# Optimization experiments

Measured on AMD Instinct MI355X. Metric: run time of the kernel, lower is better.

The kernel has to match this reference:

```python
import jax, jax.numpy as jnp
import numpy as np

EPS = 1e-8  # RMSNormMultiHead default eps (forward passes self.eps)


def rms_norm_multihead(x, weight):
    # x: (B, L, H, d); normalize over last dim in float32, then scale per (H, d)
    x32 = x.astype(jnp.float32)
    normed = x32 * jax.lax.rsqrt(jnp.mean(x32 * x32, axis=-1, keepdims=True) + EPS)
    return normed.astype(x.dtype) * weight


def setup_inputs() -> dict:
    key = jax.random.key(0)
    k0, k1, k2 = jax.random.split(key, 3)
    B, L, D, H = 2, 1024, 1024, 16
    d = D // H
    X = jax.random.normal(k0, (B, L, D), dtype=jnp.float32)
    Wq = jax.random.normal(k1, (D, D), dtype=jnp.float32) * 0.02  # q_proj weight (out, in)
    Wv = jax.random.normal(k2, (D, D), dtype=jnp.float32) * 0.02  # v_proj weight (out, in)
    q_norm_w = jnp.ones((H, d), dtype=jnp.float32)
    v_norm_w = jnp.ones((H, d), dtype=jnp.float32)
    return {"X": X, "Wq": Wq, "Wv": Wv, "q_norm_w": q_norm_w, "v_norm_w": v_norm_w}


def reference(X, Wq, Wv, q_norm_w, v_norm_w):
    B, L, D = X.shape
    H, d = q_norm_w.shape
    K = X.reshape(B, L, H, d)
    Q = rms_norm_multihead((X @ Wq.T).reshape(B, L, H, d), q_norm_w)
    V = rms_norm_multihead((X @ Wv.T).reshape(B, L, H, d), v_norm_w)
    # cumulative outer-product KV state: (B, L, H, d, e)
    W = jnp.cumsum(jnp.einsum('blhd,blhe->blhde', K, V), axis=1)
    out = jnp.einsum('blhd,blhde->blhe', Q, W).reshape(B, L, D)
    return out
```

## Files before the change

### kernel.cpp

```cpp
#include <hip/hip_runtime.h>

#define BB 2
#define LL 1024
#define DD 1024
#define HH 16
#define NC 16
#define EPSF 1e-8f

typedef __attribute__((ext_vector_type(8))) short bf16x8;
typedef __attribute__((ext_vector_type(4))) float f32x4;
typedef unsigned short u16;

static __device__ inline u16 f2bf(float f) {
    unsigned int u = __builtin_bit_cast(unsigned int, f);
    u += 0x7fff + ((u >> 16) & 1);
    return (u16)(u >> 16);
}
static __device__ inline float bf2f(u16 v) {
    unsigned int u = ((unsigned int)v) << 16;
    return __builtin_bit_cast(float, u);
}
static __device__ inline void gload_lds16(const u16* g, u16* l) {
    __builtin_amdgcn_global_load_lds((const __attribute__((address_space(1))) void*)g,
                                     (__attribute__((address_space(3))) void*)l, 16, 0, 0);
}

__global__ __launch_bounds__(256) void cvt_k(const float* __restrict__ X,
                                             const float* __restrict__ Wq,
                                             const float* __restrict__ Wv,
                                             u16* __restrict__ Xb,
                                             u16* __restrict__ Wqb,
                                             u16* __restrict__ Wvb)
{
    int i = (blockIdx.x * 256 + threadIdx.x) * 4;
    const float* s; u16* d; int off;
    if (i < 2*1024*1024)      { s = X;  d = Xb;  off = i; }
    else if (i < 3*1024*1024) { s = Wq; d = Wqb; off = i - 2*1024*1024; }
    else                      { s = Wv; d = Wvb; off = i - 3*1024*1024; }
    float4 v = *(const float4*)(s + off);
    ushort4 o;
    o.x = f2bf(v.x); o.y = f2bf(v.y); o.z = f2bf(v.z); o.w = f2bf(v.w);
    *(ushort4*)(d + off) = o;
}

__global__ __launch_bounds__(256) void gemm_fused(const u16* __restrict__ Xb,
                                                  const u16* __restrict__ Wqb,
                                                  const u16* __restrict__ Wvb,
                                                  const float* __restrict__ qw,
                                                  const float* __restrict__ vw,
                                                  u16* __restrict__ Qb,
                                                  u16* __restrict__ Vb,
                                                  u16* __restrict__ S)
{
    const int K = DD, N = DD;
    const u16* W = blockIdx.z ? Wvb : Wqb;
    const float* nw = blockIdx.z ? vw : qw;
    u16* Y = blockIdx.z ? Vb : Qb;
    __shared__ u16 As0[128 * 32], As1[128 * 32];
    __shared__ u16 Bs0[64 * 32],  Bs1[64 * 32];
    __shared__ u16 Vt[64][136];
    __shared__ u16 Kt[64][136];

    const int tid = threadIdx.x, w = tid >> 6, lane = tid & 63;
    const int quad = lane >> 4, l16 = lane & 15;
    const int m0 = blockIdx.y * 128, n0 = blockIdx.x * 64;
    const int lrow = lane >> 2;
    const int lcol = ((lane & 3) ^ ((lane >> 3) & 3)) * 8;

    const u16* gA0 = Xb + (size_t)(m0 + w*16 + lrow) * K + lcol;
    const u16* gA1 = gA0 + (size_t)64 * K;
    const u16* gB0 = W + (size_t)(n0 + w*16 + lrow) * K + lcol;
    u16* lA0_0 = &As0[(w*16) * 32];      u16* lA0_1 = &As1[(w*16) * 32];
    u16* lA1_0 = &As0[(64 + w*16) * 32]; u16* lA1_1 = &As1[(64 + w*16) * 32];
    u16* lB0_0 = &Bs0[(w*16) * 32];      u16* lB0_1 = &Bs1[(w*16) * 32];

    const int sw = (quad ^ ((l16 >> 1) & 3)) * 8;

    f32x4 acc[2][4] = {};
    for (int k0 = 0; k0 < K; k0 += 64) {
        gload_lds16(gA0 + k0,      lA0_0);
        gload_lds16(gA0 + k0 + 32, lA0_1);
        gload_lds16(gA1 + k0,      lA1_0);
        gload_lds16(gA1 + k0 + 32, lA1_1);
        gload_lds16(gB0 + k0,      lB0_0);
        gload_lds16(gB0 + k0 + 32, lB0_1);
        __syncthreads();
        #pragma unroll
        for (int hh = 0; hh < 2; ++hh) {
            const u16* Ah = hh ? As1 : As0;
            const u16* Bh = hh ? Bs1 : Bs0;
            bf16x8 af[2], bfr[4];
            #pragma unroll
            for (int i = 0; i < 2; ++i)
                af[i] = *(const bf16x8*)&Ah[(w*32 + i*16 + l16) * 32 + sw];
            #pragma unroll
            for (int j = 0; j < 4; ++j)
                bfr[j] = *(const bf16x8*)&Bh[(j*16 + l16) * 32 + sw];
            #pragma unroll
            for (int i = 0; i < 2; ++i)
                #pragma unroll
                for (int j = 0; j < 4; ++j)
                    acc[i][j] = __builtin_amdgcn_mfma_f32_16x16x32_bf16(af[i], bfr[j], acc[i][j], 0, 0, 0);
        }
        __syncthreads();
    }

    float wv4[4];
    #pragma unroll
    for (int j = 0; j < 4; ++j) wv4[j] = nw[n0 + j*16 + l16];
    #pragma unroll
    for (int i = 0; i < 2; ++i) {
        float ss[4];
        #pragma unroll
        for (int r = 0; r < 4; ++r) {
            float s = 0.f;
            #pragma unroll
            for (int j = 0; j < 4; ++j) s += acc[i][j][r] * acc[i][j][r];
            ss[r] = s;
        }
        #pragma unroll
        for (int off = 1; off < 16; off <<= 1)
            #pragma unroll
            for (int r = 0; r < 4; ++r) ss[r] += __shfl_xor(ss[r], off, 64);
        float sc[4];
        #pragma unroll
        for (int r = 0; r < 4; ++r) sc[r] = rsqrtf(ss[r] * (1.f/64.f) + EPSF);
        #pragma unroll
        for (int r = 0; r < 4; ++r) {
            u16* yp = Y + (size_t)(m0 + w*32 + i*16 + quad*4 + r) * N + n0;
            #pragma unroll
            for (int j = 0; j < 4; ++j) {
                u16 val = f2bf(acc[i][j][r] * sc[r] * wv4[j]);
                yp[j*16 + l16] = val;
                if (blockIdx.z)
                    Vt[j*16 + l16][w*32 + i*16 + quad*4 + r] = val;
            }
        }
    }

    if (blockIdx.z) {
        {
            const int row = tid >> 1, q2 = tid & 1;
            size_t gb = (size_t)(m0 + row) * DD + n0 + q2 * 32;
            u16 kk[32];
            #pragma unroll
            for (int i2 = 0; i2 < 32; i2 += 4)
                *(ushort4*)&kk[i2] = *(const ushort4*)(Xb + gb + i2);
            #pragma unroll
            for (int i2 = 0; i2 < 32; ++i2)
                Kt[q2*32 + i2][row] = kk[i2];
        }
        __syncthreads();
        const int me = (w & 1) * 32, nd = (w >> 1) * 32;
        const int b = m0 >> 10, c0 = (m0 & 1023) >> 6, h = blockIdx.x;
        const int bh = b * HH + h;
        #pragma unroll
        for (int cc = 0; cc < 2; ++cc) {
            f32x4 sacc[2][2] = {};
            #pragma unroll
            for (int k0 = 0; k0 < 64; k0 += 32) {
                bf16x8 av[2], bv[2];
                #pragma unroll
                for (int i2 = 0; i2 < 2; ++i2)
                    av[i2] = *(const bf16x8*)&Vt[me + i2*16 + l16][cc*64 + k0 + quad*8];
                #pragma unroll
                for (int j2 = 0; j2 < 2; ++j2)
                    bv[j2] = *(const bf16x8*)&Kt[nd + j2*16 + l16][cc*64 + k0 + quad*8];
                #pragma unroll
                for (int i2 = 0; i2 < 2; ++i2)
                    #pragma unroll
                    for (int j2 = 0; j2 < 2; ++j2)
                        sacc[i2][j2] = __builtin_amdgcn_mfma_f32_16x16x32_bf16(av[i2], bv[j2], sacc[i2][j2], 0, 0, 0);
            }
            u16* Sp = S + ((size_t)((bh << 4) | (c0 + cc)) << 12) + w*1024;
            #pragma unroll
            for (int i2 = 0; i2 < 2; ++i2)
                #pragma unroll
                for (int j2 = 0; j2 < 2; ++j2)
                    #pragma unroll
                    for (int r = 0; r < 4; ++r)
                        Sp[(i2*2 + j2)*256 + r*64 + lane] = f2bf(sacc[i2][j2][r]);
        }
    }
}

__global__ __launch_bounds__(256) void out_k2(const u16* __restrict__ Xb,
                                              const u16* __restrict__ Qb,
                                              const u16* __restrict__ Vb,
                                              const u16* __restrict__ S,
                                              float* __restrict__ out)
{
    const int c = 15 - (blockIdx.x & 15);
    const int bh = blockIdx.x >> 4;
    const int h = bh & 15, b = bh >> 4;
    __shared__ u16 Qs[64][72];
    __shared__ u16 Ks[64][72];
    __shared__ u16 Vt[64][72];
    __shared__ u16 St[64][72];
    const int tid = threadIdx.x;
    {
        const int row = tid >> 2, q = tid & 3;
        size_t gbase = (size_t)(b*LL + c*64 + row) * DD + h*64 + q*16;
        u16 vv[16];
        #pragma unroll
        for (int i = 0; i < 16; i += 4) {
            *(ushort4*)&Qs[row][q*16 + i] = *(const ushort4*)(Qb + gbase + i);
            *(ushort4*)&Ks[row][q*16 + i] = *(const ushort4*)(Xb + gbase + i);
            *(ushort4*)&vv[i] = *(const ushort4*)(Vb + gbase + i);
        }
        #pragma unroll
        for (int i = 0; i < 16; ++i)
            Vt[q*16 + i][row] = vv[i];
        float facc[16] = {};
        const u16* Sbase = S + ((size_t)(bh * NC) << 12);
        int cp = 0;
        for (; cp + 2 <= c; cp += 2) {
            const u16* Sc0 = Sbase + ((size_t)cp << 12);
            const u16* Sc1 = Sc0 + 4096;
            #pragma unroll
            for (int jj = 0; jj < 4; ++jj) {
                ushort4 sv0 = *(const ushort4*)(Sc0 + tid*4 + jj*1024);
                ushort4 sv1 = *(const ushort4*)(Sc1 + tid*4 + jj*1024);
                facc[jj*4+0] += bf2f(sv0.x); facc[jj*4+0] += bf2f(sv1.x);
                facc[jj*4+1] += bf2f(sv0.y); facc[jj*4+1] += bf2f(sv1.y);
                facc[jj*4+2] += bf2f(sv0.z); facc[jj*4+2] += bf2f(sv1.z);
                facc[jj*4+3] += bf2f(sv0.w); facc[jj*4+3] += bf2f(sv1.w);
            }
        }
        if (cp < c) {
            const u16* Sc = Sbase + ((size_t)cp << 12);
            #pragma unroll
            for (int jj = 0; jj < 4; ++jj) {
                ushort4 sv = *(const ushort4*)(Sc + tid*4 + jj*1024);
                facc[jj*4+0] += bf2f(sv.x);
                facc[jj*4+1] += bf2f(sv.y);
                facc[jj*4+2] += bf2f(sv.z);
                facc[jj*4+3] += bf2f(sv.w);
            }
        }
        #pragma unroll
        for (int jj = 0; jj < 4; ++jj) {
            int g = tid * 4;
            int ij = (g >> 8) & 3, r = (g >> 6) & 3, ln = g & 63;
            int e = (jj & 1)*32 + (ij >> 1)*16 + (ln >> 4)*4 + r;
            int d = (jj >> 1)*32 + (ij & 1)*16 + (ln & 15);
            ushort4 o;
            o.x = f2bf(facc[jj*4+0]);
            o.y = f2bf(facc[jj*4+1]);
            o.z = f2bf(facc[jj*4+2]);
            o.w = f2bf(facc[jj*4+3]);
            *(ushort4*)&St[e][d] = o;
        }
    }
    __syncthreads();
    const int w = tid >> 6, lane = tid & 63, quad = lane >> 4, l16 = lane & 15;
    const int mo = (w & 1) * 32, no = (w >> 1) * 32;

    f32x4 pacc[2][2] = {};
    #pragma unroll
    for (int k0 = 0; k0 < 64; k0 += 32) {
        bf16x8 aq[2], bk[2];
        #pragma unroll
        for (int i = 0; i < 2; ++i)
            aq[i] = *(const bf16x8*)&Qs[mo + i*16 + l16][k0 + quad*8];
        #pragma unroll
        for (int j = 0; j < 2; ++j)
            bk[j] = *(const bf16x8*)&Ks[no + j*16 + l16][k0 + quad*8];
        #pragma unroll
        for (int i = 0; i < 2; ++i)
            #pragma unroll
            for (int j = 0; j < 2; ++j)
                pacc[i][j] = __builtin_amdgcn_mfma_f32_16x16x32_bf16(aq[i], bk[j], pacc[i][j], 0, 0, 0);
    }
    __syncthreads();
    #pragma unroll
    for (int i = 0; i < 2; ++i)
        #pragma unroll
        for (int j = 0; j < 2; ++j)
            #pragma unroll
            for (int r = 0; r < 4; ++r) {
                int l  = mo + i*16 + quad*4 + r;
                int lp = no + j*16 + l16;
                Ks[l][lp] = (lp <= l) ? f2bf(pacc[i][j][r]) : (u16)0;
            }
    __syncthreads();

    f32x4 acc[2][2] = {};
    #pragma unroll
    for (int k0 = 0; k0 < 64; k0 += 32) {
        bf16x8 a1[2], b1[2], a2[2], b2[2];
        #pragma unroll
        for (int i = 0; i < 2; ++i) {
            a1[i] = *(const bf16x8*)&Ks[mo + i*16 + l16][k0 + quad*8];
            a2[i] = *(const bf16x8*)&Qs[mo + i*16 + l16][k0 + quad*8];
        }
        #pragma unroll
        for (int j = 0; j < 2; ++j) {
            b1[j] = *(const bf16x8*)&Vt[no + j*16 + l16][k0 + quad*8];
            b2[j] = *(const bf16x8*)&St[no + j*16 + l16][k0 + quad*8];
        }
        #pragma unroll
        for (int i = 0; i < 2; ++i)
            #pragma unroll
            for (int j = 0; j < 2; ++j) {
                acc[i][j] = __builtin_amdgcn_mfma_f32_16x16x32_bf16(a1[i], b1[j], acc[i][j], 0, 0, 0);
                acc[i][j] = __builtin_amdgcn_mfma_f32_16x16x32_bf16(a2[i], b2[j], acc[i][j], 0, 0, 0);
            }
    }
    float* op = out + (size_t)(b*LL + c*64) * DD + h*64;
    #pragma unroll
    for (int i = 0; i < 2; ++i)
        #pragma unroll
        for (int j = 0; j < 2; ++j)
            #pragma unroll
            for (int r = 0; r < 4; ++r)
                op[(size_t)(mo + i*16 + quad*4 + r) * DD + no + j*16 + l16] = acc[i][j][r];
}

extern "C" void kernel_launch(void* const* d_in, const int* in_sizes, int n_in,
                              void* d_out, int out_size, void* d_ws, size_t ws_size,
                              hipStream_t stream) {
    const float* X  = (const float*)d_in[0];
    const float* Wq = (const float*)d_in[1];
    const float* Wv = (const float*)d_in[2];
    const float* qw = (const float*)d_in[3];
    const float* vw = (const float*)d_in[4];
    float* out = (float*)d_out;

    u16* Xb  = (u16*)d_ws;
    u16* Wqb = Xb  + (size_t)2*1024*1024;
    u16* Wvb = Wqb + (size_t)1024*1024;
    u16* Qb  = Wvb + (size_t)1024*1024;
    u16* Vb  = Qb  + (size_t)2*1024*1024;
    u16* S   = Vb  + (size_t)2*1024*1024;

    cvt_k<<<4096, 256, 0, stream>>>(X, Wq, Wv, Xb, Wqb, Wvb);
    gemm_fused<<<dim3(16, 16, 2), 256, 0, stream>>>(Xb, Wqb, Wvb, qw, vw, Qb, Vb, S);
    out_k2<<<BB*HH*NC, 256, 0, stream>>>(Xb, Qb, Vb, S, out);
}
```

Baseline: 99.01 us.

## Double-buffer GEMM K-loop with async LDS prefetch and unroll state prefix sum

The fused Q/V projection GEMM now keeps two LDS buffers with a wider 64-element k row layout and a new XOR swizzle. The next k-tile is prefetched via global_load_lds while MFMAs run on the current one, so there is one barrier per iteration instead of two. The LDS used by the epilogue transposes is aliased onto the same shared buffer to hold LDS at 48KB. Separately, the chunk-state prefix accumulation loads four chunks at a time to put more memory loads in flight.

New measurement: 96.96 us. 1.02x faster.

```diff
diff --git a/kernel.cpp b/kernel.cpp
--- a/kernel.cpp
+++ b/kernel.cpp
@@ -56,54 +56,65 @@
     const u16* W = blockIdx.z ? Wvb : Wqb;
     const float* nw = blockIdx.z ? vw : qw;
     u16* Y = blockIdx.z ? Vb : Qb;
-    __shared__ u16 As0[128 * 32], As1[128 * 32];
-    __shared__ u16 Bs0[64 * 32],  Bs1[64 * 32];
-    __shared__ u16 Vt[64][136];
-    __shared__ u16 Kt[64][136];
+
+    __shared__ alignas(16) char smem[49152];
+    u16* Ab = (u16*)smem;
+    u16* Bb = (u16*)(smem + 32768);
 
     const int tid = threadIdx.x, w = tid >> 6, lane = tid & 63;
     const int quad = lane >> 4, l16 = lane & 15;
     const int m0 = blockIdx.y * 128, n0 = blockIdx.x * 64;
-    const int lrow = lane >> 2;
-    const int lcol = ((lane & 3) ^ ((lane >> 3) & 3)) * 8;
-
-    const u16* gA0 = Xb + (size_t)(m0 + w*16 + lrow) * K + lcol;
-    const u16* gA1 = gA0 + (size_t)64 * K;
-    const u16* gB0 = W + (size_t)(n0 + w*16 + lrow) * K + lcol;
-    u16* lA0_0 = &As0[(w*16) * 32];      u16* lA0_1 = &As1[(w*16) * 32];
-    u16* lA1_0 = &As0[(64 + w*16) * 32]; u16* lA1_1 = &As1[(64 + w*16) * 32];
-    u16* lB0_0 = &Bs0[(w*16) * 32];      u16* lB0_1 = &Bs1[(w*16) * 32];
-
-    const int sw = (quad ^ ((l16 >> 1) & 3)) * 8;
+
+    const int lr8 = lane >> 3;
+    const int lc8 = (lane & 7) ^ lr8;
+    const u16* gA = Xb + (size_t)(m0 + w*32 + lr8) * K + lc8 * 8;
+    const u16* gB = W  + (size_t)(n0 + w*16 + lr8) * K + lc8 * 8;
 
     f32x4 acc[2][4] = {};
-    for (int k0 = 0; k0 < K; k0 += 64) {
-        gload_lds16(gA0 + k0,      lA0_0);
-        gload_lds16(gA0 + k0 + 32, lA0_1);
-        gload_lds16(gA1 + k0,      lA1_0);
-        gload_lds16(gA1 + k0 + 32, lA1_1);
-        gload_lds16(gB0 + k0,      lB0_0);
-        gload_lds16(gB0 + k0 + 32, lB0_1);
-        __syncthreads();
+
+    auto stage = [&](int buf, int k0) {
+        u16* As = Ab + buf * (128*64);
+        u16* Bs = Bb + buf * (64*64);
+        #pragma unroll
+        for (int q = 0; q < 4; ++q)
+            gload_lds16(gA + k0 + (size_t)q*8*K, As + (w*32 + q*8)*64);
+        #pragma unroll
+        for (int q = 0; q < 2; ++q)
+            gload_lds16(gB + k0 + (size_t)q*8*K, Bs + (w*16 + q*8)*64);
+    };
+    auto compute = [&](int buf) {
+        const u16* As = Ab + buf * (128*64);
+        const u16* Bs = Bb + buf * (64*64);
         #pragma unroll
         for (int hh = 0; hh < 2; ++hh) {
-            const u16* Ah = hh ? As1 : As0;
-            const u16* Bh = hh ? Bs1 : Bs0;
+            const int co = (((hh << 2) | quad) ^ (l16 & 7)) * 8;
             bf16x8 af[2], bfr[4];
             #pragma unroll
             for (int i = 0; i < 2; ++i)
-                af[i] = *(const bf16x8*)&Ah[(w*32 + i*16 + l16) * 32 + sw];
+                af[i] = *(const bf16x8*)&As[(w*32 + i*16 + l16) * 64 + co];
             #pragma unroll
             for (int j = 0; j < 4; ++j)
-                bfr[j] = *(const bf16x8*)&Bh[(j*16 + l16) * 32 + sw];
+                bfr[j] = *(const bf16x8*)&Bs[(j*16 + l16) * 64 + co];
             #pragma unroll
             for (int i = 0; i < 2; ++i)
                 #pragma unroll
                 for (int j = 0; j < 4; ++j)
                     acc[i][j] = __builtin_amdgcn_mfma_f32_16x16x32_bf16(af[i], bfr[j], acc[i][j], 0, 0, 0);
         }
+    };
+
+    stage(0, 0);
+    __syncthreads();
+    int cur = 0;
+    for (int k0 = 0; k0 < K; k0 += 64) {
+        if (k0 + 64 < K) stage(cur ^ 1, k0 + 64);
+        compute(cur);
         __syncthreads();
-    }
+        cur ^= 1;
+    }
+
+    u16 (*Vt)[136] = (u16 (*)[136])smem;
+    u16 (*Kt)[136] = (u16 (*)[136])(smem + 17408);
 
     float wv4[4];
     #pragma unroll
@@ -214,20 +225,24 @@
         float facc[16] = {};
         const u16* Sbase = S + ((size_t)(bh * NC) << 12);
         int cp = 0;
-        for (; cp + 2 <= c; cp += 2) {
-            const u16* Sc0 = Sbase + ((size_t)cp << 12);
-            const u16* Sc1 = Sc0 + 4096;
-            #pragma unroll
-            for (int jj = 0; jj < 4; ++jj) {
-                ushort4 sv0 = *(const ushort4*)(Sc0 + tid*4 + jj*1024);
-                ushort4 sv1 = *(const ushort4*)(Sc1 + tid*4 + jj*1024);
-                facc[jj*4+0] += bf2f(sv0.x); facc[jj*4+0] += bf2f(sv1.x);
-                facc[jj*4+1] += bf2f(sv0.y); facc[jj*4+1] += bf2f(sv1.y);
-                facc[jj*4+2] += bf2f(sv0.z); facc[jj*4+2] += bf2f(sv1.z);
-                facc[jj*4+3] += bf2f(sv0.w); facc[jj*4+3] += bf2f(sv1.w);
-            }
-        }
-        if (cp < c) {
+        for (; cp + 4 <= c; cp += 4) {
+            ushort4 sv[4][4];
+            #pragma unroll
+            for (int u = 0; u < 4; ++u)
+                #pragma unroll
+                for (int jj = 0; jj < 4; ++jj)
+                    sv[u][jj] = *(const ushort4*)(Sbase + ((size_t)(cp + u) << 12) + tid*4 + jj*1024);
+            #pragma unroll
+            for (int u = 0; u < 4; ++u)
+                #pragma unroll
+                for (int jj = 0; jj < 4; ++jj) {
+                    facc[jj*4+0] += bf2f(sv[u][jj].x);
+                    facc[jj*4+1] += bf2f(sv[u][jj].y);
+                    facc[jj*4+2] += bf2f(sv[u][jj].z);
+                    facc[jj*4+3] += bf2f(sv[u][jj].w);
+                }
+        }
+        for (; cp < c; ++cp) {
             const u16* Sc = Sbase + ((size_t)cp << 12);
             #pragma unroll
             for (int jj = 0; jj < 4; ++jj) {
```
